# Performance work log

Measured on AMD Instinct MI355X. Metric: run time of the kernel, lower is better.

Reference implementation:

```python
import jax, jax.numpy as jnp
import numpy as np

H = 16        # query heads
K = 4         # kv heads (GQA)
D = 128       # head_dim
HID = 2048    # hidden_size
T = 2048      # num tokens (single prefill sequence, causal)
THETA = 10000.0


def setup_inputs() -> dict:
    key = jax.random.key(0)
    k1, k2, k3 = jax.random.split(key, 3)
    hidden_states = jax.random.normal(k1, (T, HID), dtype=jnp.float32)
    position_ids = jnp.arange(T, dtype=jnp.int32)
    Wqkv = jax.random.normal(k2, (HID, (H + 2 * K) * D), dtype=jnp.float32) * 0.02
    Wo = jax.random.normal(k3, (H * D, HID), dtype=jnp.float32) * 0.02
    return {"hidden_states": hidden_states, "position_ids": position_ids,
            "Wqkv": Wqkv, "Wo": Wo}


def _rope_neox(x, pos):
    # x: [T, heads, D]; neox style: rotate halves
    half = D // 2
    inv_freq = 1.0 / (THETA ** (jnp.arange(0, D, 2, dtype=jnp.float32) / D))  # [D/2]
    ang = pos.astype(jnp.float32)[:, None] * inv_freq                          # [T, D/2]
    cos = jnp.cos(ang)[:, None, :]
    sin = jnp.sin(ang)[:, None, :]
    x1, x2 = x[..., :half], x[..., half:]
    return jnp.concatenate([x1 * cos - x2 * sin, x2 * cos + x1 * sin], axis=-1)


def reference(hidden_states, position_ids, Wqkv, Wo):
    t = hidden_states.shape[0]
    qkv = hidden_states @ Wqkv                                   # [T, (H+2K)*D]
    q = qkv[:, : H * D].reshape(t, H, D)
    k = qkv[:, H * D : (H + K) * D].reshape(t, K, D)
    v = qkv[:, (H + K) * D :].reshape(t, K, D)
    q = _rope_neox(q, position_ids)
    k = _rope_neox(k, position_ids)
    # GQA: expand kv heads to H
    rep = H // K
    k = jnp.repeat(k, rep, axis=1)                               # [T, H, D]
    v = jnp.repeat(v, rep, axis=1)
    scale = D ** -0.5
    scores = jnp.einsum('qhd,khd->hqk', q, k) * scale            # [H, T, T]
    causal = jnp.arange(t)[:, None] >= jnp.arange(t)[None, :]    # [T, T]
    scores = jnp.where(causal[None], scores, jnp.finfo(scores.dtype).min)
    probs = jax.nn.softmax(scores, axis=-1)
    ctx = jnp.einsum('hqk,khd->qhd', probs, v).reshape(t, H * D)  # [T, H*D]
    return ctx @ Wo                                              # [T, HID]
```

## Files before the change

### kernel.cpp

```cpp
#include <hip/hip_runtime.h>
#include <hip/hip_bf16.h>
#include <stdint.h>

typedef __hip_bfloat16 bf16;
typedef __attribute__((ext_vector_type(8))) short bh8;
typedef __attribute__((ext_vector_type(4))) float f32x4;

#define MFMA16(a, b, c) __builtin_amdgcn_mfma_f32_16x16x32_bf16((a), (b), (c), 0, 0, 0)

typedef const __attribute__((address_space(1))) void* gas1_t;
typedef __attribute__((address_space(3))) void* las3_t;

__device__ __forceinline__ void gload_lds16(const void* g, void* l) {
  __builtin_amdgcn_global_load_lds((gas1_t)g, (las3_t)l, 16, 0, 0);
}

__device__ __forceinline__ float bfu2f(unsigned short u) {
  union { unsigned int i; float f; } c;
  c.i = (unsigned int)u << 16;
  return c.f;
}

__global__ __launch_bounds__(256) void cast_f32_bf16(const float* __restrict__ x,
                                                     bf16* __restrict__ y, int n4) {
  int i = blockIdx.x * 256 + threadIdx.x;
  if (i >= n4) return;
  float4 v = ((const float4*)x)[i];
  union { ushort4 u; bf16 b[4]; } o;
  o.b[0] = __float2bfloat16(v.x);
  o.b[1] = __float2bfloat16(v.y);
  o.b[2] = __float2bfloat16(v.z);
  o.b[3] = __float2bfloat16(v.w);
  ((ushort4*)y)[i] = o.u;
}

__global__ __launch_bounds__(256) void transpose_cast(const float* __restrict__ W,
                                                      bf16* __restrict__ WT, int R, int C) {
  __shared__ float tile[32][33];
  const int tx = threadIdx.x & 31, ty = threadIdx.x >> 5;
  const int bx = blockIdx.x, by = blockIdx.y;
#pragma unroll
  for (int p = 0; p < 4; ++p)
    tile[ty + p * 8][tx] = W[(long)(by * 32 + ty + p * 8) * C + bx * 32 + tx];
  __syncthreads();
#pragma unroll
  for (int p = 0; p < 4; ++p)
    WT[(long)(bx * 32 + ty + p * 8) * R + by * 32 + tx] = __float2bfloat16(tile[tx][ty + p * 8]);
}

template <bool BF16OUT>
__global__ __launch_bounds__(256) void gemm_bt_sk(const bf16* __restrict__ A,
                                                  const bf16* __restrict__ BT,
                                                  void* __restrict__ C0, void* __restrict__ C1,
                                                  int M, int N, int Kd, int nKs) {
  __shared__ bf16 As[2][128 * 64];
  __shared__ bf16 Bs[2][128 * 64];
  const int tid = threadIdx.x, lane = tid & 63, wid = tid >> 6;
  const int wr = wid >> 1, wc = wid & 1;
  const int bx = blockIdx.x, by = blockIdx.y, z = blockIdx.z;

  f32x4 acc[4][4];
#pragma unroll
  for (int m = 0; m < 4; ++m)
#pragma unroll
    for (int n = 0; n < 4; ++n)
#pragma unroll
      for (int r = 0; r < 4; ++r) acc[m][n][r] = 0.0f;

  const long Abase = (long)(by * 128) * Kd;
  const long Bbase = (long)(bx * 128) * Kd;
  const int lr = lane & 15, lh = lane >> 4;
  const int k00 = z * nKs * 64;

#define G_STAGE(BUF, KT)                                                                   \
  {                                                                                        \
    const int k0 = k00 + (KT) * 64;                                                        \
    _Pragma("unroll") for (int i = 0; i < 4; ++i) {                                        \
      const int cb = i * 256 + wid * 64;                                                   \
      const int c = cb + lane;                                                             \
      const int row = c >> 3, s = c & 7;                                                   \
      gload_lds16(A + Abase + (long)row * Kd + k0 + (s ^ (row & 7)) * 8,                   \
                  (char*)As[BUF] + cb * 16);                                               \
      gload_lds16(BT + Bbase + (long)row * Kd + k0 + (s ^ (row & 7)) * 8,                  \
                  (char*)Bs[BUF] + cb * 16);                                               \
    }                                                                                      \
  }

  G_STAGE(0, 0);
  __syncthreads();
  int cur = 0;
  for (int kt = 0; kt < nKs; ++kt) {
    if (kt + 1 < nKs) G_STAGE(cur ^ 1, kt + 1);
    const char* Ab = (const char*)As[cur];
    const char* Bb = (const char*)Bs[cur];
#pragma unroll
    for (int kk = 0; kk < 2; ++kk) {
      bh8 af[4], bfv[4];
#pragma unroll
      for (int m = 0; m < 4; ++m)
        af[m] = *(const bh8*)(Ab + (((wr * 64 + m * 16 + lr) * 128 + kk * 64 + lh * 16) ^
                                    ((lr & 7) << 4)));
#pragma unroll
      for (int n = 0; n < 4; ++n)
        bfv[n] = *(const bh8*)(Bb + (((wc * 64 + n * 16 + lr) * 128 + kk * 64 + lh * 16) ^
                                     ((lr & 7) << 4)));
#pragma unroll
      for (int m = 0; m < 4; ++m)
#pragma unroll
        for (int n = 0; n < 4; ++n) acc[m][n] = MFMA16(af[m], bfv[n], acc[m][n]);
    }
    __syncthreads();
    cur ^= 1;
  }
#undef G_STAGE

  const int r0 = by * 128 + wr * 64, c0i = bx * 128 + wc * 64;
  const int lrow = lh * 4;
  if (BF16OUT) {
    bf16* P = (bf16*)(z == 0 ? C0 : C1);
#pragma unroll
    for (int m = 0; m < 4; ++m)
#pragma unroll
      for (int n = 0; n < 4; ++n)
#pragma unroll
        for (int r = 0; r < 4; ++r)
          P[(long)(r0 + m * 16 + lrow + r) * N + c0i + n * 16 + lr] =
              __float2bfloat16(acc[m][n][r]);
  } else {
    float* P = (float*)(z == 0 ? C0 : C1);
#pragma unroll
    for (int m = 0; m < 4; ++m)
#pragma unroll
      for (int n = 0; n < 4; ++n)
#pragma unroll
        for (int r = 0; r < 4; ++r)
          P[(long)(r0 + m * 16 + lrow + r) * N + c0i + n * 16 + lr] = acc[m][n][r];
  }
}

__global__ __launch_bounds__(256) void out_reduce(float* __restrict__ out,
                                                  const float* __restrict__ p1, int n4) {
  int i = blockIdx.x * 256 + threadIdx.x;
  if (i >= n4) return;
  float4 a = ((const float4*)out)[i];
  float4 b = ((const float4*)p1)[i];
  a.x += b.x; a.y += b.y; a.z += b.z; a.w += b.w;
  ((float4*)out)[i] = a;
}

__global__ __launch_bounds__(256) void rope_split(const bf16* __restrict__ P0,
                                                  const bf16* __restrict__ P1,
                                                  const int* __restrict__ pos_ids,
                                                  bf16* __restrict__ Qb, bf16* __restrict__ Kb,
                                                  bf16* __restrict__ VbT) {
  __shared__ float lcs[64], lsn[64];
  const int t = blockIdx.x;
  const int tid = threadIdx.x;
  const float pos = (float)pos_ids[t];
  const float qscale = 0.08838834764831845f;
  const ushort* r0 = (const ushort*)(P0 + (long)t * 3072);
  const ushort* r1 = (const ushort*)(P1 + (long)t * 3072);

  if (tid < 64) {
    const float inv = exp2f((float)tid * -0.2076205059304594f);
    float s, c;
    __sincosf(pos * inv, &s, &c);
    lcs[tid] = c;
    lsn[tid] = s;
  }
  __syncthreads();

  for (int i = tid; i < 512; i += 256) {
    const int kvh = i >> 7, d = i & 127;
    const float v = bfu2f(r0[2560 + i]) + bfu2f(r1[2560 + i]);
    VbT[(long)(kvh * 128 + d) * 2048 + t] = __float2bfloat16(v);
  }
  for (int i = tid; i < 1280; i += 256) {
    const int hh = i >> 6, d = i & 63;
    const float c = lcs[d], s = lsn[d];
    const float x1 = bfu2f(r0[hh * 128 + d]) + bfu2f(r1[hh * 128 + d]);
    const float x2 = bfu2f(r0[hh * 128 + d + 64]) + bfu2f(r1[hh * 128 + d + 64]);
    const float o1 = x1 * c - x2 * s, o2 = x2 * c + x1 * s;
    if (hh < 16) {
      Qb[(long)t * 2048 + hh * 128 + d] = __float2bfloat16(o1 * qscale);
      Qb[(long)t * 2048 + hh * 128 + d + 64] = __float2bfloat16(o2 * qscale);
    } else {
      Kb[t * 512 + (hh - 16) * 128 + d] = __float2bfloat16(o1);
      Kb[t * 512 + (hh - 16) * 128 + d + 64] = __float2bfloat16(o2);
    }
  }
}

__global__ __launch_bounds__(256, 2) void attn_partial(const bf16* __restrict__ Qb,
                                                       const bf16* __restrict__ Kb,
                                                       const bf16* __restrict__ VbT,
                                                       bf16* __restrict__ Pctx,
                                                       float* __restrict__ ML) {
  const int h = blockIdx.x;
  const int qb = 31 - blockIdx.y;
  const int z = blockIdx.z;
  const int kh = h >> 2;
  const int tid = threadIdx.x, lane = tid & 63, w = tid >> 6;
  const int pid = (h * 32 + qb) * 2 + z;

  const int nt = qb + 1;
  const int half = (nt + 1) >> 1;
  const int kt0 = z * half;
  const int kt1 = (z == 0) ? half : nt;

  if (kt0 >= kt1) {
    if (tid < 64) {
      ML[pid * 128 + tid] = -1e30f;
      ML[pid * 128 + 64 + tid] = 0.0f;
    }
    ushort4 z4 = make_ushort4(0, 0, 0, 0);
    ushort4* pz = (ushort4*)(Pctx + (long)pid * 8192);
    for (int j = tid; j < 2048; j += 256) pz[j] = z4;
    return;
  }

  __shared__ bf16 Kl[2][64 * 128];
  __shared__ bf16 Vt[2][128 * 64];

  const int lr = lane & 15, lh = lane >> 4;
  const int q0w = qb * 64 + w * 16;

#define KV_STAGE(BUF, KT)                                                                  \
  {                                                                                        \
    const long Kbase = ((long)((KT) * 64) * 4 + kh) * 128;                                 \
    _Pragma("unroll") for (int i = 0; i < 4; ++i) {                                        \
      const int cb = i * 256 + w * 64;                                                     \
      const int c = cb + lane;                                                             \
      const int krow = c >> 4, s = c & 15;                                                 \
      const int g = s ^ ((krow & 3) | ((krow & 8) >> 1));                                  \
      gload_lds16(Kb + Kbase + (long)krow * 512 + g * 8, (char*)Kl[BUF] + cb * 16);        \
    }                                                                                      \
    const long Vbase = (long)kh * 128 * 2048 + (KT) * 64;                                  \
    _Pragma("unroll") for (int i = 0; i < 4; ++i) {                                        \
      const int cb = i * 256 + w * 64;                                                     \
      const int c = cb + lane;                                                             \
      const int vrow = c >> 3, s = c & 7;                                                  \
      gload_lds16(VbT + Vbase + (long)vrow * 2048 + (s ^ (vrow & 7)) * 8,                  \
                  (char*)Vt[BUF] + cb * 16);                                               \
    }                                                                                      \
  }

  bh8 qf[4];
#pragma unroll
  for (int dc = 0; dc < 4; ++dc)
    qf[dc] = *(const bh8*)&Qb[(long)(q0w + lr) * 2048 + h * 128 + dc * 32 + lh * 8];

  f32x4 ctx[8];
#pragma unroll
  for (int i = 0; i < 8; ++i)
#pragma unroll
    for (int r = 0; r < 4; ++r) ctx[i][r] = 0.0f;
  float mrun = -1e30f, lrun = 0.0f;

  KV_STAGE(0, kt0);
  __syncthreads();
  int cur = 0;
  for (int kt = kt0; kt < kt1; ++kt) {
    if (kt + 1 < kt1) KV_STAGE(cur ^ 1, kt + 1);
    const char* Kc = (const char*)Kl[cur];
    const char* Vc = (const char*)Vt[cur];

    f32x4 S[2][2];
#pragma unroll
    for (int kc = 0; kc < 2; ++kc)
#pragma unroll
      for (int b = 0; b < 2; ++b) {
#pragma unroll
        for (int r = 0; r < 4; ++r) S[kc][b][r] = 0.0f;
        const int key = kc * 32 + ((lr >> 2) << 3) + b * 4 + (lr & 3);
        const int kbase = key * 256 + lh * 16;
#pragma unroll
        for (int dc = 0; dc < 4; ++dc) {
          bh8 kf = *(const bh8*)(Kc + ((kbase + dc * 64) ^ ((lr & 7) << 4)));
          S[kc][b] = MFMA16(kf, qf[dc], S[kc][b]);
        }
      }

    if (kt == qb) {
      const int qg = q0w + lr;
#pragma unroll
      for (int kc = 0; kc < 2; ++kc)
#pragma unroll
        for (int b = 0; b < 2; ++b)
#pragma unroll
          for (int r = 0; r < 4; ++r) {
            const int kg = kt * 64 + kc * 32 + lh * 8 + b * 4 + r;
            if (kg > qg) S[kc][b][r] = -1e30f;
          }
    }

    float pm = -1e30f;
#pragma unroll
    for (int kc = 0; kc < 2; ++kc)
#pragma unroll
      for (int b = 0; b < 2; ++b)
#pragma unroll
        for (int r = 0; r < 4; ++r) pm = fmaxf(pm, S[kc][b][r]);
    pm = fmaxf(pm, __shfl_xor(pm, 16, 64));
    pm = fmaxf(pm, __shfl_xor(pm, 32, 64));

    if (__any(pm > mrun + 4.0f)) {
      const float mnew = fmaxf(mrun, pm);
      const float alpha = __expf(mrun - mnew);
      mrun = mnew;
      lrun *= alpha;
      float a4[4];
#pragma unroll
      for (int r = 0; r < 4; ++r) a4[r] = __shfl(alpha, lh * 4 + r, 64);
#pragma unroll
      for (int i = 0; i < 8; ++i)
#pragma unroll
        for (int r = 0; r < 4; ++r) ctx[i][r] *= a4[r];
    }

    bh8 pa[2];
#pragma unroll
    for (int kc = 0; kc < 2; ++kc) {
      union { bh8 v; bf16 e[8]; } pk;
#pragma unroll
      for (int b = 0; b < 2; ++b)
#pragma unroll
        for (int r = 0; r < 4; ++r) {
          const float p = __expf(S[kc][b][r] - mrun);
          lrun += p;
          pk.e[b * 4 + r] = __float2bfloat16(p);
        }
      pa[kc] = pk.v;
    }

#pragma unroll
    for (int kc = 0; kc < 2; ++kc)
#pragma unroll
      for (int dblk = 0; dblk < 8; ++dblk) {
        const int vrow = dblk * 16 + lr;
        const int voff = (vrow * 128 + kc * 64 + lh * 16) ^ ((lr & 7) << 4);
        bh8 vb = *(const bh8*)(Vc + voff);
        ctx[dblk] = MFMA16(pa[kc], vb, ctx[dblk]);
      }

    __syncthreads();
    cur ^= 1;
  }
#undef KV_STAGE

  float l = lrun;
  l += __shfl_xor(l, 16, 64);
  l += __shfl_xor(l, 32, 64);
  if (lh == 0) {
    ML[pid * 128 + w * 16 + lr] = mrun;
    ML[pid * 128 + 64 + w * 16 + lr] = l;
  }
#pragma unroll
  for (int dblk = 0; dblk < 8; ++dblk)
#pragma unroll
    for (int r = 0; r < 4; ++r)
      Pctx[(long)pid * 8192 + (w * 16 + lh * 4 + r) * 128 + dblk * 16 + lr] =
          __float2bfloat16(ctx[dblk][r]);
}

__global__ __launch_bounds__(256) void attn_merge(const bf16* __restrict__ Pctx,
                                                  const float* __restrict__ ML,
                                                  bf16* __restrict__ out) {
  const int h = blockIdx.x, qb = blockIdx.y;
  const int tid = threadIdx.x;
  const int r = tid >> 2, seg = tid & 3;
  const int pid0 = (h * 32 + qb) * 2;
  const float m0 = ML[pid0 * 128 + r], l0 = ML[pid0 * 128 + 64 + r];
  const float m1 = ML[pid0 * 128 + 128 + r], l1 = ML[pid0 * 128 + 192 + r];
  const float m = fmaxf(m0, m1);
  float a0 = __expf(m0 - m), a1 = __expf(m1 - m);
  const float inv = 1.0f / (l0 * a0 + l1 * a1);
  a0 *= inv;
  a1 *= inv;
  const ushort* p0 = (const ushort*)(Pctx + (long)pid0 * 8192 + r * 128 + seg * 32);
  const ushort* p1 = p0 + 8192;
  bf16* o = out + (long)(qb * 64 + r) * 2048 + h * 128 + seg * 32;
#pragma unroll
  for (int j = 0; j < 4; ++j) {
    union { bh8 v; ushort s[8]; } v0, v1;
    v0.v = *(const bh8*)(p0 + j * 8);
    v1.v = *(const bh8*)(p1 + j * 8);
    union { ushort4 u; bf16 b[4]; } o0, o1;
#pragma unroll
    for (int e = 0; e < 4; ++e) {
      o0.b[e] = __float2bfloat16(bfu2f(v0.s[e]) * a0 + bfu2f(v1.s[e]) * a1);
      o1.b[e] = __float2bfloat16(bfu2f(v0.s[e + 4]) * a0 + bfu2f(v1.s[e + 4]) * a1);
    }
    *(ushort4*)(o + j * 8) = o0.u;
    *(ushort4*)(o + j * 8 + 4) = o1.u;
  }
}

extern "C" void kernel_launch(void* const* d_in, const int* in_sizes, int n_in,
                              void* d_out, int out_size, void* d_ws, size_t ws_size,
                              hipStream_t stream) {
  const float* hs = (const float*)d_in[0];
  const int* pos = (const int*)d_in[1];
  const float* Wqkv = (const float*)d_in[2];
  const float* Wo = (const float*)d_in[3];
  char* ws = (char*)d_ws;

  bf16* hsb = (bf16*)(ws);
  bf16* ctx = (bf16*)(ws);
  bf16* wqkvT = (bf16*)(ws + (8l << 20));
  bf16* Qb = (bf16*)(ws + (8l << 20));
  bf16* Kb = (bf16*)(ws + (16l << 20));
  bf16* VbT = (bf16*)(ws + (18l << 20));
  bf16* woT = (bf16*)(ws + (20l << 20));
  bf16* qkvP0 = (bf16*)(ws + (28l << 20));
  bf16* qkvP1 = (bf16*)(ws + (40l << 20));
  bf16* Pctx = (bf16*)(ws + (28l << 20));
  float* ML = (float*)(ws + (44l << 20));
  float* outP1 = (float*)(ws + (28l << 20));

  cast_f32_bf16<<<4096, 256, 0, stream>>>(hs, hsb, 2048 * 2048 / 4);
  transpose_cast<<<dim3(3072 / 32, 2048 / 32), 256, 0, stream>>>(Wqkv, wqkvT, 2048, 3072);
  transpose_cast<<<dim3(2048 / 32, 2048 / 32), 256, 0, stream>>>(Wo, woT, 2048, 2048);
  gemm_bt_sk<true><<<dim3(24, 16, 2), 256, 0, stream>>>(hsb, wqkvT, qkvP0, qkvP1,
                                                        2048, 3072, 2048, 16);
  rope_split<<<2048, 256, 0, stream>>>(qkvP0, qkvP1, pos, Qb, Kb, VbT);
  attn_partial<<<dim3(16, 32, 2), 256, 0, stream>>>(Qb, Kb, VbT, Pctx, ML);
  attn_merge<<<dim3(16, 32), 256, 0, stream>>>(Pctx, ML, ctx);
  gemm_bt_sk<false><<<dim3(16, 16, 2), 256, 0, stream>>>(ctx, woT, d_out, outP1,
                                                         2048, 2048, 2048, 16);
  out_reduce<<<4096, 256, 0, stream>>>((float*)d_out, outP1, 2048 * 2048 / 4);
}
```

Baseline: 225.7 us.

## Fuse prep kernels, remap GEMM blocks across XCDs, use explicit vmcnt waits

Merges the bf16 cast and the two weight transpose-casts into one launch so two kernel launches go away. Remaps GEMM workgroup IDs so consecutive tiles land on the same XCD, which should improve L2 reuse. In the GEMM and attention loops, replaces __syncthreads with explicit s_waitcnt vmcnt plus raw s_barrier, so the current buffer is waited on while the next stage's loads stay in flight. The hardcoded vmcnt of 8 must match the number of loads issued per stage, or the code reads stale LDS.

```diff
diff --git a/kernel.cpp b/kernel.cpp
--- a/kernel.cpp
+++ b/kernel.cpp
@@ -7,6 +7,7 @@
 typedef __attribute__((ext_vector_type(4))) float f32x4;
 
 #define MFMA16(a, b, c) __builtin_amdgcn_mfma_f32_16x16x32_bf16((a), (b), (c), 0, 0, 0)
+#define VMCNT(N) asm volatile("s_waitcnt vmcnt(" #N ")" ::: "memory")
 
 typedef const __attribute__((address_space(1))) void* gas1_t;
 typedef __attribute__((address_space(3))) void* las3_t;
@@ -21,24 +22,35 @@
   return c.f;
 }
 
-__global__ __launch_bounds__(256) void cast_f32_bf16(const float* __restrict__ x,
-                                                     bf16* __restrict__ y, int n4) {
-  int i = blockIdx.x * 256 + threadIdx.x;
-  if (i >= n4) return;
-  float4 v = ((const float4*)x)[i];
-  union { ushort4 u; bf16 b[4]; } o;
-  o.b[0] = __float2bfloat16(v.x);
-  o.b[1] = __float2bfloat16(v.y);
-  o.b[2] = __float2bfloat16(v.z);
-  o.b[3] = __float2bfloat16(v.w);
-  ((ushort4*)y)[i] = o.u;
-}
-
-__global__ __launch_bounds__(256) void transpose_cast(const float* __restrict__ W,
-                                                      bf16* __restrict__ WT, int R, int C) {
+__global__ __launch_bounds__(256) void prep(const float* __restrict__ hs, bf16* __restrict__ hsb,
+                                            const float* __restrict__ Wqkv,
+                                            bf16* __restrict__ wqkvT,
+                                            const float* __restrict__ Wo,
+                                            bf16* __restrict__ woT) {
+  const int b = blockIdx.x, tid = threadIdx.x;
+  if (b < 4096) {
+    const int i = b * 256 + tid;
+    float4 v = ((const float4*)hs)[i];
+    union { ushort4 u; bf16 bb[4]; } o;
+    o.bb[0] = __float2bfloat16(v.x);
+    o.bb[1] = __float2bfloat16(v.y);
+    o.bb[2] = __float2bfloat16(v.z);
+    o.bb[3] = __float2bfloat16(v.w);
+    ((ushort4*)hsb)[i] = o.u;
+    return;
+  }
   __shared__ float tile[32][33];
-  const int tx = threadIdx.x & 31, ty = threadIdx.x >> 5;
-  const int bx = blockIdx.x, by = blockIdx.y;
+  const float* W;
+  bf16* WT;
+  int bx, by, R, C;
+  if (b < 4096 + 6144) {
+    const int bb = b - 4096;
+    bx = bb % 96; by = bb / 96; R = 2048; C = 3072; W = Wqkv; WT = wqkvT;
+  } else {
+    const int bb = b - 10240;
+    bx = bb % 64; by = bb / 64; R = 2048; C = 2048; W = Wo; WT = woT;
+  }
+  const int tx = tid & 31, ty = tid >> 5;
 #pragma unroll
   for (int p = 0; p < 4; ++p)
     tile[ty + p * 8][tx] = W[(long)(by * 32 + ty + p * 8) * C + bx * 32 + tx];
@@ -57,7 +69,12 @@
   __shared__ bf16 Bs[2][128 * 64];
   const int tid = threadIdx.x, lane = tid & 63, wid = tid >> 6;
   const int wr = wid >> 1, wc = wid & 1;
-  const int bx = blockIdx.x, by = blockIdx.y, z = blockIdx.z;
+
+  const int gx = gridDim.x, gy = gridDim.y;
+  const int nwg = gx * gy * gridDim.z;
+  const int orig = (blockIdx.z * gy + blockIdx.y) * gx + blockIdx.x;
+  const int widq = (orig & 7) * (nwg >> 3) + (orig >> 3);
+  const int bx = widq % gx, by = (widq / gx) % gy, z = widq / (gx * gy);
 
   f32x4 acc[4][4];
 #pragma unroll
@@ -87,10 +104,16 @@
   }
 
   G_STAGE(0, 0);
-  __syncthreads();
   int cur = 0;
   for (int kt = 0; kt < nKs; ++kt) {
-    if (kt + 1 < nKs) G_STAGE(cur ^ 1, kt + 1);
+    if (kt + 1 < nKs) {
+      G_STAGE(cur ^ 1, kt + 1);
+      VMCNT(8);
+    } else {
+      VMCNT(0);
+    }
+    __builtin_amdgcn_sched_barrier(0);
+    __builtin_amdgcn_s_barrier();
     const char* Ab = (const char*)As[cur];
     const char* Bb = (const char*)Bs[cur];
 #pragma unroll
@@ -109,7 +132,7 @@
 #pragma unroll
         for (int n = 0; n < 4; ++n) acc[m][n] = MFMA16(af[m], bfv[n], acc[m][n]);
     }
-    __syncthreads();
+    __builtin_amdgcn_s_barrier();
     cur ^= 1;
   }
 #undef G_STAGE
@@ -258,10 +281,16 @@
   float mrun = -1e30f, lrun = 0.0f;
 
   KV_STAGE(0, kt0);
-  __syncthreads();
   int cur = 0;
   for (int kt = kt0; kt < kt1; ++kt) {
-    if (kt + 1 < kt1) KV_STAGE(cur ^ 1, kt + 1);
+    if (kt + 1 < kt1) {
+      KV_STAGE(cur ^ 1, kt + 1);
+      VMCNT(8);
+    } else {
+      VMCNT(0);
+    }
+    __builtin_amdgcn_sched_barrier(0);
+    __builtin_amdgcn_s_barrier();
     const char* Kc = (const char*)Kl[cur];
     const char* Vc = (const char*)Vt[cur];
 
@@ -343,7 +372,7 @@
         ctx[dblk] = MFMA16(pa[kc], vb, ctx[dblk]);
       }
 
-    __syncthreads();
+    __builtin_amdgcn_s_barrier();
     cur ^= 1;
   }
 #undef KV_STAGE
@@ -418,9 +447,7 @@
   float* ML = (float*)(ws + (44l << 20));
   float* outP1 = (float*)(ws + (28l << 20));
 
-  cast_f32_bf16<<<4096, 256, 0, stream>>>(hs, hsb, 2048 * 2048 / 4);
-  transpose_cast<<<dim3(3072 / 32, 2048 / 32), 256, 0, stream>>>(Wqkv, wqkvT, 2048, 3072);
-  transpose_cast<<<dim3(2048 / 32, 2048 / 32), 256, 0, stream>>>(Wo, woT, 2048, 2048);
+  prep<<<14336, 256, 0, stream>>>(hs, hsb, Wqkv, wqkvT, Wo, woT);
   gemm_bt_sk<true><<<dim3(24, 16, 2), 256, 0, stream>>>(hsb, wqkvT, qkvP0, qkvP1,
                                                         2048, 3072, 2048, 16);
   rope_split<<<2048, 256, 0, stream>>>(qkvP0, qkvP1, pos, Qb, Kb, VbT);
```

New measurement: 222.5 us. No clear change (-1.4%).
